# Kernel optimization log

Hardware: AMD Instinct MI355X
Metric: run time of the kernel (lower is better)

The kernel has to match this reference:

```python
import jax, jax.numpy as jnp
import numpy as np
from jax import lax

SPAN = 11
K = 2 * SPAN + 1          # 23 -> 529 offsets
SIG_RGB = 0.1
SIG_XY = 6.0
LAM = 0.15
B, C, H, W = 2, 3, 160, 160


def _patches(x):
    """x: (N, C, H, W) -> (N, C, K, K, H, W), zero-padded.
    patch[di, dj] at pixel (i, j) equals x[i + di - SPAN, j + dj - SPAN],
    matching the torch module's shifted-slice double loop (dx = di - SPAN)."""
    n, c, h, w = x.shape
    xp = jnp.pad(x, ((0, 0), (0, 0), (SPAN, SPAN), (SPAN, SPAN)))

    def get(off):
        di = off // K
        dj = off % K
        return lax.dynamic_slice(xp, (0, 0, di, dj), (n, c, h, w))

    p = jax.vmap(get)(jnp.arange(K * K))              # (K*K, N, C, H, W)
    return p.reshape(K, K, n, c, h, w).transpose(2, 3, 0, 1, 4, 5)


def setup_inputs() -> dict:
    key = jax.random.key(0)
    k1, k2, k3, k4, k5 = jax.random.split(key, 5)
    logit = jax.random.normal(k1, (B, C, H, W), jnp.float32)
    target = jax.random.randint(k2, (B, H, W), 0, C)
    # small-magnitude image so exp(-0.5*(x - patch/0.1)^2) does not fully underflow
    image = jax.random.uniform(k3, (B, 3, H, W), jnp.float32) * 0.1
    source_map = (jax.random.uniform(k4, (B, 1, H, W)) > 0.5).astype(jnp.float32)
    destination_map = (jax.random.uniform(k5, (B, H, W)) > 0.5).astype(jnp.float32)
    return dict(logit=logit, target=target, image=image,
                source_map=source_map, destination_map=destination_map)


def _gcrf(image, y_hat, source_map, m_dst):
    b, c, h, w = y_hat.shape
    img_p = _patches(image)                                  # (B,3,K,K,H,W)
    valid = _patches(jnp.ones((1, 1, h, w), image.dtype))[0, 0]  # (K,K,H,W) in-bounds mask
    # NOTE: faithful to source bug: only the shifted feature is divided by sigma
    drgb = image[:, :, None, None] - img_p / SIG_RGB
    k_rgb = jnp.exp(-0.5 * jnp.sum(drgb * drgb, axis=1))     # (B,K,K,H,W)
    ii, jj = jnp.meshgrid(jnp.arange(h, dtype=image.dtype),
                          jnp.arange(w, dtype=image.dtype), indexing='ij')
    idx = jnp.stack([ii, jj])[None]                          # (1,2,H,W)
    idx_p = _patches(idx)[0]                                 # (2,K,K,H,W)
    dxy = idx[0][:, None, None] - idx_p / SIG_XY
    k_xy = jnp.exp(-0.5 * jnp.sum(dxy * dxy, axis=0))        # (K,K,H,W)
    kmat = (k_rgb + k_xy[None]) * valid[None]                # out-of-bounds offsets stay 0
    m_src = _patches(source_map)[:, 0]                       # (B,K,K,H,W)
    Kg = kmat * m_src * m_dst[:, None, None]                 # gated kernel
    U = _patches(y_hat)                                      # (B,C,K,K,H,W)
    Egy = jnp.einsum('bcijhw,bijhw->bchw', U, Kg)            # sum over window
    temp = jnp.einsum('bchw,bdhw->bcd', Egy, y_hat)          # (B,C,C)
    Moff = 1.0 - jnp.eye(c, dtype=y_hat.dtype)               # off-diagonal compatibility
    return jnp.sum(Moff * temp) / (b * h * w)


def reference(logit, target, image, source_map, destination_map):
    y_hat = jax.nn.softmax(logit, axis=1)
    m_dst = 1.0 - destination_map
    L_gcrf = _gcrf(image, y_hat, source_map, m_dst)
    logp = jax.nn.log_softmax(logit, axis=1)
    L_ce = -jnp.take_along_axis(logp, target[:, None], axis=1)[:, 0]  # (B,H,W)
    L_ce = jnp.mean(L_ce * destination_map)
    return L_ce + LAM * L_gcrf
```

## Files before the change

### kernel.cpp

```cpp
#include <hip/hip_runtime.h>

#define Bn 2
#define Cn 3
#define Hn 160
#define Wn 160
#define SPANc 11
#define Kc 23
#define HWn (Hn * Wn)
#define PW 182
#define PP (PW * PW)
#define LAMc 0.15f
#define INVN (1.0f / (float)(Bn * HWn))
#define TJ 32
#define Gc 4
#define TI 32
#define CEXP (-0.72134752f)
#define CX   (14.42695041f)
#define CA   (0.72134752f)
#define NPREP ((Bn * PP + 255) / 256)
#define NCELL 64
#define CELLSTRIDE 64

__device__ __forceinline__ float wave_reduce64(float v) {
#pragma unroll
    for (int off = 32; off > 0; off >>= 1) v += __shfl_down(v, off, 64);
    return v;
}

__device__ __forceinline__ unsigned int bf16pk(float a, float b) {
    unsigned int ua = __float_as_uint(a), ub = __float_as_uint(b);
    ua += 0x7fffu + ((ua >> 16) & 1u);
    ub += 0x7fffu + ((ub >> 16) & 1u);
    return (ua & 0xffff0000u) | (ub >> 16);
}

__global__ __launch_bounds__(256) void prep_kernel(
    const float* __restrict__ logit, const int* __restrict__ target,
    const float* __restrict__ image, const float* __restrict__ srcmap,
    const float* __restrict__ dstmap, uint4* __restrict__ gU4,
    float4* __restrict__ cvec, float* __restrict__ pc, float* __restrict__ cells)
{
    int idx = blockIdx.x * 256 + threadIdx.x;
    float ce = 0.0f;
    if (idx < NCELL) cells[idx * CELLSTRIDE] = 0.0f;
    if (idx < Bn * PP) {
        int b   = idx / PP;
        int rem = idx - b * PP;
        int ip  = rem / PW;
        int jp  = rem - ip * PW;
        int i = ip - SPANc, j = jp - SPANc;
        if ((unsigned)i < (unsigned)Hn && (unsigned)j < (unsigned)Wn) {
            int r = i * Wn + j;
            int p = b * HWn + r;
            const float* lg = logit + (size_t)b * Cn * HWn + r;
            float l0 = lg[0], l1 = lg[HWn], l2 = lg[2 * HWn];
            float m = fmaxf(l0, fmaxf(l1, l2));
            float e0 = __expf(l0 - m), e1 = __expf(l1 - m), e2 = __expf(l2 - m);
            float s = e0 + e1 + e2;
            float inv = 1.0f / s;
            float y0 = e0 * inv, y1 = e1 * inv, y2 = e2 * inv;
            float lse = m + __logf(s);

            const float* im = image + (size_t)b * 3 * HWn + r;
            float p0 = im[0], p1 = im[HWn], p2 = im[2 * HWn];
            float sv = srcmap[p];
            float dv = dstmap[p];

            float B = (p0 * p0 + p1 * p1 + p2 * p2) * (100.0f * CA);
            gU4[idx] = make_uint4(bf16pk(p0, p1), bf16pk(p2, -B),
                                  bf16pk(sv * y0, sv * y1), bf16pk(sv * y2, 0.0f));

            float md = LAMc * (1.0f - dv) * INVN;
            cvec[p] = make_float4(md * (1.0f - y0), md * (1.0f - y1),
                                  md * (1.0f - y2), 0.0f);

            int t = target[p];
            float lt = (t == 0) ? l0 : ((t == 1) ? l1 : l2);
            ce = (lse - lt) * dv * INVN;
        } else {
            gU4[idx] = make_uint4(0u, 0u, 0u, 0u);
        }
    }

    float v = wave_reduce64(ce);
    __shared__ float wsum[4];
    int tid = threadIdx.x;
    if ((tid & 63) == 0) wsum[tid >> 6] = v;
    __syncthreads();
    if (tid == 0) pc[blockIdx.x] = wsum[0] + wsum[1] + wsum[2] + wsum[3];
}

template<bool XY>
__device__ __forceinline__ void tap(float p0, float p1, float p2, float mB,
                                    float q0, float q1, float q2,
                                    float c0s, float c1s, float c2s, float mA,
                                    bool xy_on, float dy2, float dxv,
                                    float& e0, float& e1, float& e2)
{
    float e = fmaf(c0s, p0, fmaf(c1s, p1, fmaf(c2s, p2, mB)));
    float k;
    if constexpr (XY) {
        k = __builtin_amdgcn_exp2f(e + mA);
        if (xy_on) k += __builtin_amdgcn_exp2f(fmaf(dxv, dxv, dy2) * CEXP);
    } else {
        k = __builtin_amdgcn_exp2f(e);
    }
    e0 = fmaf(k, q0, e0);
    e1 = fmaf(k, q1, e1);
    e2 = fmaf(k, q2, e2);
}

template<bool XY>
__device__ __forceinline__ void row_taps(uint4 ru, int r,
    const float* c0s, const float* c1s, const float* c2s, const float* mA,
    bool xy_on, float dy2, float fi0, float eg[Gc][3], int clo, int chi)
{
    float p0 = __uint_as_float(ru.x & 0xffff0000u);
    float p1 = __uint_as_float(ru.x << 16);
    float p2 = __uint_as_float(ru.y & 0xffff0000u);
    float mB = __uint_as_float(ru.y << 16);
    float q0 = __uint_as_float(ru.z & 0xffff0000u);
    float q1 = __uint_as_float(ru.z << 16);
    float q2 = __uint_as_float(ru.w & 0xffff0000u);
    float dxb = XY ? (fi0 - (fi0 + (float)(r - SPANc)) * (1.0f / 6.0f)) : 0.0f;
#pragma unroll
    for (int c = 0; c < Gc; ++c) {
        if (c < clo || c > chi) continue;
        tap<XY>(p0, p1, p2, mB, q0, q1, q2, c0s[c], c1s[c], c2s[c], mA[c],
                xy_on, dy2, dxb + (float)c, eg[c][0], eg[c][1], eg[c][2]);
    }
}

template<bool XY>
__device__ __forceinline__ void window_loop(
    const uint4* __restrict__ gbase,
    const float* c0s, const float* c1s, const float* c2s, const float* mA,
    bool xy_on, float dy2, float fi0, float eg[Gc][3])
{
#pragma unroll
    for (int r = 0; r < 3; ++r) {
        row_taps<XY>(gbase[(size_t)r * PW], r, c0s, c1s, c2s, mA,
                     xy_on, dy2, fi0, eg, 0, r);
    }
#pragma unroll 2
    for (int r = 3; r <= 22; ++r) {
        row_taps<XY>(gbase[(size_t)r * PW], r, c0s, c1s, c2s, mA,
                     xy_on, dy2, fi0, eg, 0, 3);
    }
#pragma unroll
    for (int r = 23; r <= 25; ++r) {
        row_taps<XY>(gbase[(size_t)r * PW], r, c0s, c1s, c2s, mA,
                     xy_on, dy2, fi0, eg, r - 22, 3);
    }
}

__global__ __launch_bounds__(256, 5) void gcrf_kernel(
    const uint4* __restrict__ gU4, const float4* __restrict__ cvec,
    float* __restrict__ cells)
{
    int tx = threadIdx.x;
    int ty = threadIdx.y;
    int tid = ty * TJ + tx;
    int jx = blockIdx.x;
    int j  = jx * TJ + tx;
    int by = blockIdx.y;
    int b  = by / 5;
    int it = by - b * 5;
    int i0g = it * TI + ty * Gc;
    int dj = blockIdx.z;

    const uint4* gbase = gU4 + (size_t)b * PP + (size_t)i0g * PW
                             + (size_t)(jx * TJ + dj) + tx;
    const uint4* gC = gU4 + (size_t)b * PP + (size_t)(i0g + SPANc) * PW
                          + (size_t)(j + SPANc);

    bool isxy = (jx == 0 && it == 0);

    float c0s[Gc], c1s[Gc], c2s[Gc], mA[Gc], kAe[Gc];
#pragma unroll
    for (int c = 0; c < Gc; ++c) {
        uint4 cu = gC[(size_t)c * PW];
        float cc0 = __uint_as_float(cu.x & 0xffff0000u);
        float cc1 = __uint_as_float(cu.x << 16);
        float cc2 = __uint_as_float(cu.y & 0xffff0000u);
        c0s[c] = cc0 * CX; c1s[c] = cc1 * CX; c2s[c] = cc2 * CX;
        mA[c] = -CA * fmaf(cc0, cc0, fmaf(cc1, cc1, cc2 * cc2));
        kAe[c] = isxy ? 1.0f : __builtin_amdgcn_exp2f(mA[c]);
    }

    bool xy_on = (j < 16) && (i0g < 16);
    float dy = (float)j - (float)(j + dj - SPANc) * (1.0f / 6.0f);
    float dy2 = dy * dy;
    float fi0 = (float)i0g;

    float eg[Gc][3];
#pragma unroll
    for (int c = 0; c < Gc; ++c) { eg[c][0] = 0.f; eg[c][1] = 0.f; eg[c][2] = 0.f; }

    if (isxy) {
        window_loop<true>(gbase, c0s, c1s, c2s, mA, xy_on, dy2, fi0, eg);
    } else {
        window_loop<false>(gbase, c0s, c1s, c2s, mA, false, dy2, fi0, eg);
    }

    const float4* cv = cvec + ((size_t)b * HWn + (size_t)i0g * Wn + j);
    float contrib = 0.0f;
#pragma unroll
    for (int c = 0; c < Gc; ++c) {
        float4 t = cv[(size_t)c * Wn];
        float d = eg[c][0] * t.x + eg[c][1] * t.y + eg[c][2] * t.z;
        contrib = fmaf(kAe[c], d, contrib);
    }

    float v = wave_reduce64(contrib);
    __shared__ float wsum[4];
    if ((tid & 63) == 0) wsum[tid >> 6] = v;
    __syncthreads();
    if (tid == 0) {
        int bflat = (blockIdx.z * gridDim.y + blockIdx.y) * gridDim.x + blockIdx.x;
        atomicAdd(cells + (size_t)(bflat & (NCELL - 1)) * CELLSTRIDE,
                  wsum[0] + wsum[1] + wsum[2] + wsum[3]);
    }
}

__global__ __launch_bounds__(64) void finalize_kernel(
    const float* __restrict__ cells, const float* __restrict__ pc,
    float* __restrict__ out)
{
    int t = threadIdx.x;
    float s = cells[(size_t)t * CELLSTRIDE];
    for (int k = t; k < NPREP; k += 64) s += pc[k];
    float v = wave_reduce64(s);
    if (t == 0) out[0] = v;
}

extern "C" void kernel_launch(void* const* d_in, const int* in_sizes, int n_in,
                              void* d_out, int out_size, void* d_ws, size_t ws_size,
                              hipStream_t stream)
{
    const float* logit  = (const float*)d_in[0];
    const int*   target = (const int*)d_in[1];
    const float* image  = (const float*)d_in[2];
    const float* srcmap = (const float*)d_in[3];
    const float* dstmap = (const float*)d_in[4];
    float* out = (float*)d_out;

    const size_t NRECG = (size_t)Bn * PP;
    float*  pc    = (float*)((char*)d_ws + 256);
    float*  cells = (float*)((char*)d_ws + 4096);
    uint4*  gU4   = (uint4*)((char*)d_ws + 4096 + 16384);
    float4* cvec  = (float4*)((char*)d_ws + 4096 + 16384 + NRECG * 16);

    prep_kernel<<<NPREP, 256, 0, stream>>>(logit, target, image, srcmap, dstmap,
                                           gU4, cvec, pc, cells);
    dim3 grid(Wn / TJ, (Hn / TI) * Bn, Kc);
    dim3 blk(TJ, 8);
    gcrf_kernel<<<grid, blk, 0, stream>>>(gU4, cvec, cells);
    finalize_kernel<<<1, 64, 0, stream>>>(cells, pc, out);
}
```

Baseline: 79.39 us.

## Stage padded tile in LDS and sweep three column offsets per block

Each block now loads a (TI+22)x(TJ+2) tile of packed records into shared memory once and reuses it across three column offsets (dj), instead of reading global memory per tap for a single dj. The row group per thread is halved (Gc 4→2, TI 32→16), which doubles the grid rows, and the z dimension shrinks from 23 to 8 groups. This targets redundant global/L2 traffic. In exchange it adds about 14KB of LDS per block, a barrier, and a serial dj loop, which may lower occupancy and also reduces the reuse of center values across rows.

```diff
diff --git a/kernel.cpp b/kernel.cpp
--- a/kernel.cpp
+++ b/kernel.cpp
@@ -12,8 +12,13 @@
 #define LAMc 0.15f
 #define INVN (1.0f / (float)(Bn * HWn))
 #define TJ 32
-#define Gc 4
-#define TI 32
+#define Gc 2
+#define TI 16
+#define DJW 3
+#define NDJG 8
+#define TROW (TI + Kc - 1)
+#define TCOL (TJ + DJW - 1 + 0)
+#define NREC (TROW * TCOL)
 #define CEXP (-0.72134752f)
 #define CX   (14.42695041f)
 #define CA   (0.72134752f)
@@ -132,25 +137,27 @@
 }
 
 template<bool XY>
-__device__ __forceinline__ void window_loop(
-    const uint4* __restrict__ gbase,
+__device__ __forceinline__ void window_sweep(
+    const uint4* sU4, int ty, int tx, int j, int djg,
     const float* c0s, const float* c1s, const float* c2s, const float* mA,
-    bool xy_on, float dy2, float fi0, float eg[Gc][3])
-{
-#pragma unroll
-    for (int r = 0; r < 3; ++r) {
-        row_taps<XY>(gbase[(size_t)r * PW], r, c0s, c1s, c2s, mA,
-                     xy_on, dy2, fi0, eg, 0, r);
-    }
+    bool xy_on, float fi0, float eg[Gc][3])
+{
+#pragma unroll 1
+    for (int l = 0; l < DJW; ++l) {
+        int dj = djg * DJW + l;
+        if (dj >= Kc) break;
+        float dy = XY ? ((float)j - (float)(j + dj - SPANc) * (1.0f / 6.0f)) : 0.0f;
+        float dy2 = dy * dy;
+        int lbase = (ty * Gc) * TCOL + tx + l;
+        row_taps<XY>(sU4[lbase], 0, c0s, c1s, c2s, mA,
+                     xy_on, dy2, fi0, eg, 0, 0);
 #pragma unroll 2
-    for (int r = 3; r <= 22; ++r) {
-        row_taps<XY>(gbase[(size_t)r * PW], r, c0s, c1s, c2s, mA,
-                     xy_on, dy2, fi0, eg, 0, 3);
-    }
-#pragma unroll
-    for (int r = 23; r <= 25; ++r) {
-        row_taps<XY>(gbase[(size_t)r * PW], r, c0s, c1s, c2s, mA,
-                     xy_on, dy2, fi0, eg, r - 22, 3);
+        for (int r = 1; r <= 22; ++r) {
+            row_taps<XY>(sU4[lbase + r * TCOL], r, c0s, c1s, c2s, mA,
+                         xy_on, dy2, fi0, eg, 0, 1);
+        }
+        row_taps<XY>(sU4[lbase + 23 * TCOL], 23, c0s, c1s, c2s, mA,
+                     xy_on, dy2, fi0, eg, 1, 1);
     }
 }
 
@@ -158,24 +165,33 @@
     const uint4* __restrict__ gU4, const float4* __restrict__ cvec,
     float* __restrict__ cells)
 {
+    __shared__ uint4 sU4[NREC];
+
     int tx = threadIdx.x;
     int ty = threadIdx.y;
     int tid = ty * TJ + tx;
     int jx = blockIdx.x;
     int j  = jx * TJ + tx;
     int by = blockIdx.y;
-    int b  = by / 5;
-    int it = by - b * 5;
+    int b  = by / 10;
+    int it = by - b * 10;
     int i0g = it * TI + ty * Gc;
-    int dj = blockIdx.z;
-
-    const uint4* gbase = gU4 + (size_t)b * PP + (size_t)i0g * PW
-                             + (size_t)(jx * TJ + dj) + tx;
+    int djg = blockIdx.z;
+
+    int cbase = jx * TJ + djg * DJW;
+    int ccmax = (PW - 1) - cbase;
+    size_t g0 = (size_t)b * PP + (size_t)(it * TI) * PW + cbase;
+    for (int n = tid; n < NREC; n += 256) {
+        int rr = n / TCOL, cc = n - rr * TCOL;
+        int ccl = (cc < ccmax) ? cc : ccmax;
+        sU4[n] = gU4[g0 + (size_t)rr * PW + ccl];
+    }
+    __syncthreads();
+
+    bool isxy = (jx == 0 && it == 0);
+
     const uint4* gC = gU4 + (size_t)b * PP + (size_t)(i0g + SPANc) * PW
                           + (size_t)(j + SPANc);
-
-    bool isxy = (jx == 0 && it == 0);
-
     float c0s[Gc], c1s[Gc], c2s[Gc], mA[Gc], kAe[Gc];
 #pragma unroll
     for (int c = 0; c < Gc; ++c) {
@@ -189,8 +205,6 @@
     }
 
     bool xy_on = (j < 16) && (i0g < 16);
-    float dy = (float)j - (float)(j + dj - SPANc) * (1.0f / 6.0f);
-    float dy2 = dy * dy;
     float fi0 = (float)i0g;
 
     float eg[Gc][3];
@@ -198,9 +212,9 @@
     for (int c = 0; c < Gc; ++c) { eg[c][0] = 0.f; eg[c][1] = 0.f; eg[c][2] = 0.f; }
 
     if (isxy) {
-        window_loop<true>(gbase, c0s, c1s, c2s, mA, xy_on, dy2, fi0, eg);
+        window_sweep<true>(sU4, ty, tx, j, djg, c0s, c1s, c2s, mA, xy_on, fi0, eg);
     } else {
-        window_loop<false>(gbase, c0s, c1s, c2s, mA, false, dy2, fi0, eg);
+        window_sweep<false>(sU4, ty, tx, j, djg, c0s, c1s, c2s, mA, false, fi0, eg);
     }
 
     const float4* cv = cvec + ((size_t)b * HWn + (size_t)i0g * Wn + j);
@@ -253,7 +267,7 @@
 
     prep_kernel<<<NPREP, 256, 0, stream>>>(logit, target, image, srcmap, dstmap,
                                            gU4, cvec, pc, cells);
-    dim3 grid(Wn / TJ, (Hn / TI) * Bn, Kc);
+    dim3 grid(Wn / TJ, (Hn / TI) * Bn, NDJG);
     dim3 blk(TJ, 8);
     gcrf_kernel<<<grid, blk, 0, stream>>>(gU4, cvec, cells);
     finalize_kernel<<<1, 64, 0, stream>>>(cells, pc, out);
```

Result: no change. 80.42 us (+1.3%).
